# Optimization experiments

Hardware: AMD Instinct MI355X
Metric: run time of the kernel (lower is better)

The kernel has to match this reference:

```python
import jax, jax.numpy as jnp
import numpy as np

B, T, D, H = 2, 4096, 768, 12
HD = D // H  # head_dim = 64


def setup_inputs() -> dict:
    key = jax.random.key(0)
    ks = jax.random.split(key, 6)
    s = 0.02
    return {
        "x": jax.random.normal(ks[0], (B, T, D), dtype=jnp.float32),
        "Wq": jax.random.normal(ks[1], (D, D), dtype=jnp.float32) * s,
        "Wk": jax.random.normal(ks[2], (D, D), dtype=jnp.float32) * s,
        "Wv": jax.random.normal(ks[3], (D, D), dtype=jnp.float32) * s,
        "Wo": jax.random.normal(ks[4], (D, D), dtype=jnp.float32) * s,
        "bo": jnp.zeros((D,), dtype=jnp.float32),
    }


def reference(x, Wq, Wk, Wv, Wo, bo):
    b, t, d = x.shape
    # QKV projections (no bias), reshape to [B, H, T, HD]
    def heads(w):
        return (x @ w.T).reshape(b, t, H, HD).transpose(0, 2, 1, 3)
    q, k, v = heads(Wq), heads(Wk), heads(Wv)
    scores = jnp.einsum("bhqd,bhkd->bhqk", q, k)  # [B,H,T,T]
    causal = jnp.tril(jnp.ones((t, t), dtype=bool))
    scores = jnp.where(causal, scores, -jnp.inf)
    attn = jax.nn.softmax(scores / jnp.sqrt(jnp.float32(HD)), axis=-1)
    ctx = jnp.einsum("bhqk,bhkd->bhqd", attn, v)  # [B,H,T,HD]
    ctx = ctx.transpose(0, 2, 1, 3).reshape(b, t, d)
    return ctx @ Wo.T + bo
```

## Files before the change

kernel.cpp:

```cpp
#include <hip/hip_runtime.h>
#include <hip/hip_bf16.h>
#include <cstdint>
#include <cstddef>

#define B_  2
#define T_  4096
#define D_  768
#define H_  12
#define HD_ 64
#define M_  (B_*T_)

#define SCL 0.18033688f

typedef __bf16 bf16x8 __attribute__((ext_vector_type(8)));
typedef float  f32x4  __attribute__((ext_vector_type(4)));
using bf16 = __hip_bfloat16;

__device__ inline float fexp2(float x) {
  float r; asm("v_exp_f32 %0, %1" : "=v"(r) : "v"(x)); return r;
}
__device__ inline uint32_t fu(float x) { union { float f; uint32_t u; } c; c.f = x; return c.u; }
__device__ inline uint32_t pktr(float a, float b) {
  return __builtin_amdgcn_perm(fu(b), fu(a), 0x07060302);
}
#define GLD16(g, l) __builtin_amdgcn_global_load_lds( \
    (const __attribute__((address_space(1))) uint32_t*)(const void*)(g), \
    (__attribute__((address_space(3))) uint32_t*)(void*)(l), 16, 0, 0)

__global__ void cvt_all(const float* __restrict__ x,
                        const float* __restrict__ w0, const float* __restrict__ w1,
                        const float* __restrict__ w2, const float* __restrict__ w3,
                        bf16* __restrict__ xd,
                        bf16* __restrict__ d0, bf16* __restrict__ d1,
                        bf16* __restrict__ d2, bf16* __restrict__ d3) {
  int blk = blockIdx.x;
  const float* s; bf16* d; int i;
  if (blk < 6144) {
    s = x; d = xd; i = blk * 256 + threadIdx.x;
  } else {
    int q = blk - 6144, which = q / 576, rb = q % 576;
    switch (which) {
      case 0: s = w0; d = d0; break;
      case 1: s = w1; d = d1; break;
      case 2: s = w2; d = d2; break;
      default: s = w3; d = d3; break;
    }
    i = rb * 256 + threadIdx.x;
  }
  float4 v = ((const float4*)s)[i];
  union { bf16 o[4]; uint2 u; } pk;
  pk.o[0] = __float2bfloat16(v.x); pk.o[1] = __float2bfloat16(v.y);
  pk.o[2] = __float2bfloat16(v.z); pk.o[3] = __float2bfloat16(v.w);
  *(uint2*)(d + 4 * (size_t)i) = pk.u;
}

__global__ __launch_bounds__(256) void gemm_qkv(const bf16* __restrict__ x,
                                                const bf16* __restrict__ W0,
                                                const bf16* __restrict__ W1,
                                                const bf16* __restrict__ W2,
                                                bf16* __restrict__ O0,
                                                bf16* __restrict__ O1,
                                                bf16* __restrict__ O2t) {
  __shared__ bf16 As[2][4096];
  __shared__ bf16 Bs[2][4096];
  const int flat = blockIdx.x;
  const int by = flat / 18;
  const int rr = flat % 18;
  const int z  = rr / 6;
  const int bx = rr % 6;
  const bf16* Wz = (z == 0) ? W0 : ((z == 1) ? W1 : W2);
  const char* Ap; const char* Bp; int a0, b0;
  if (z == 2) { Ap = (const char*)x;  a0 = by * 128; Bp = (const char*)Wz; b0 = bx * 128; }
  else        { Ap = (const char*)Wz; a0 = bx * 128; Bp = (const char*)x;  b0 = by * 128; }
  const int t = threadIdx.x;
  const int w = t >> 6, lane = t & 63;
  const int wa = (w >> 1) * 64, wb = (w & 1) * 64;
  const int mi = lane & 15, qd = lane >> 4;

  int aoff[2], boff[2];
  #pragma unroll
  for (int i = 0; i < 2; ++i) {
    int L = i * 256 + t;
    int row = L >> 2, sl = L & 3, c = sl ^ (row & 3);
    aoff[i] = (a0 + row) * 1536 + c * 16;
    boff[i] = (b0 + row) * 1536 + c * 16;
  }
  const int fsw = (qd ^ (mi & 3)) * 8;

  f32x4 acc[4][4] = {};

  #pragma unroll
  for (int i = 0; i < 2; ++i) {
    GLD16(Ap + aoff[i], &As[0][i * 2048 + w * 512]);
    GLD16(Bp + boff[i], &Bs[0][i * 2048 + w * 512]);
  }

  for (int kk = 0; kk < 24; ++kk) {
    __syncthreads();
    const int par = kk & 1;
    if (kk + 1 < 24) {
      const int np = par ^ 1, kb = (kk + 1) * 64;
      #pragma unroll
      for (int i = 0; i < 2; ++i) {
        GLD16(Ap + aoff[i] + kb, &As[np][i * 2048 + w * 512]);
        GLD16(Bp + boff[i] + kb, &Bs[np][i * 2048 + w * 512]);
      }
    }
    bf16x8 af[4], bfr[4];
    #pragma unroll
    for (int at = 0; at < 4; ++at)
      af[at] = *(const bf16x8*)&As[par][(wa + at * 16 + mi) * 32 + fsw];
    #pragma unroll
    for (int bt = 0; bt < 4; ++bt)
      bfr[bt] = *(const bf16x8*)&Bs[par][(wb + bt * 16 + mi) * 32 + fsw];
    #pragma unroll
    for (int at = 0; at < 4; ++at)
      #pragma unroll
      for (int bt = 0; bt < 4; ++bt)
        acc[at][bt] = __builtin_amdgcn_mfma_f32_16x16x32_bf16(af[at], bfr[bt], acc[at][bt], 0, 0, 0);
  }

  if (z == 2) {
    #pragma unroll
    for (int at = 0; at < 4; ++at)
      #pragma unroll
      for (int bt = 0; bt < 4; ++bt) {
        int gr = a0 + wa + at * 16 + qd * 4;
        int gc = b0 + wb + bt * 16 + mi;
        union { bf16 o[4]; uint2 u; } pk;
        #pragma unroll
        for (int r = 0; r < 4; ++r) pk.o[r] = __float2bfloat16(acc[at][bt][r]);
        int bb = gr >> 12, tt = gr & 4095;
        *(uint2*)(O2t + (size_t)bb * 768 * 4096 + (size_t)gc * 4096 + tt) = pk.u;
      }
  } else {
    const float scl = (z == 1) ? SCL : 1.0f;
    bf16* Ob = (z == 0) ? O0 : O1;
    #pragma unroll
    for (int at = 0; at < 4; ++at)
      #pragma unroll
      for (int bt = 0; bt < 4; ++bt) {
        int f0  = a0 + wa + at * 16 + qd * 4;
        int tkn = b0 + wb + bt * 16 + mi;
        union { bf16 o[4]; uint2 u; } pk;
        #pragma unroll
        for (int r = 0; r < 4; ++r) pk.o[r] = __float2bfloat16(acc[at][bt][r] * scl);
        *(uint2*)(Ob + (size_t)tkn * 768 + f0) = pk.u;
      }
  }
}

__global__ __launch_bounds__(256) void gemm_out(const bf16* __restrict__ ctx,
                                                const bf16* __restrict__ Wo,
                                                float* __restrict__ Cf,
                                                const float* __restrict__ bias) {
  __shared__ bf16 As[2][4096];
  __shared__ bf16 Bs[2][4096];
  const int flat = blockIdx.x;
  const int by = flat / 6, bx = flat % 6;
  const char* Ap = (const char*)Wo;  const int a0 = bx * 128;
  const char* Bp = (const char*)ctx; const int b0 = by * 128;
  const int t = threadIdx.x;
  const int w = t >> 6, lane = t & 63;
  const int wa = (w >> 1) * 64, wb = (w & 1) * 64;
  const int mi = lane & 15, qd = lane >> 4;

  int aoff[2], boff[2];
  #pragma unroll
  for (int i = 0; i < 2; ++i) {
    int L = i * 256 + t;
    int row = L >> 2, sl = L & 3, c = sl ^ (row & 3);
    aoff[i] = (a0 + row) * 1536 + c * 16;
    boff[i] = (b0 + row) * 1536 + c * 16;
  }
  const int fsw = (qd ^ (mi & 3)) * 8;

  f32x4 acc[4][4] = {};

  #pragma unroll
  for (int i = 0; i < 2; ++i) {
    GLD16(Ap + aoff[i], &As[0][i * 2048 + w * 512]);
    GLD16(Bp + boff[i], &Bs[0][i * 2048 + w * 512]);
  }

  for (int kk = 0; kk < 24; ++kk) {
    __syncthreads();
    const int par = kk & 1;
    if (kk + 1 < 24) {
      const int np = par ^ 1, kb = (kk + 1) * 64;
      #pragma unroll
      for (int i = 0; i < 2; ++i) {
        GLD16(Ap + aoff[i] + kb, &As[np][i * 2048 + w * 512]);
        GLD16(Bp + boff[i] + kb, &Bs[np][i * 2048 + w * 512]);
      }
    }
    bf16x8 af[4], bfr[4];
    #pragma unroll
    for (int at = 0; at < 4; ++at)
      af[at] = *(const bf16x8*)&As[par][(wa + at * 16 + mi) * 32 + fsw];
    #pragma unroll
    for (int bt = 0; bt < 4; ++bt)
      bfr[bt] = *(const bf16x8*)&Bs[par][(wb + bt * 16 + mi) * 32 + fsw];
    #pragma unroll
    for (int at = 0; at < 4; ++at)
      #pragma unroll
      for (int bt = 0; bt < 4; ++bt)
        acc[at][bt] = __builtin_amdgcn_mfma_f32_16x16x32_bf16(af[at], bfr[bt], acc[at][bt], 0, 0, 0);
  }

  #pragma unroll
  for (int at = 0; at < 4; ++at)
    #pragma unroll
    for (int bt = 0; bt < 4; ++bt) {
      int f0  = a0 + wa + at * 16 + qd * 4;
      int tkn = b0 + wb + bt * 16 + mi;
      float4 bv = *(const float4*)&bias[f0];
      float4 o;
      o.x = acc[at][bt][0] + bv.x; o.y = acc[at][bt][1] + bv.y;
      o.z = acc[at][bt][2] + bv.z; o.w = acc[at][bt][3] + bv.w;
      *(float4*)&Cf[(size_t)tkn * 768 + f0] = o;
    }
}

__global__ __launch_bounds__(512, 4) void flash_attn(const bf16* __restrict__ Q,
                                                     const bf16* __restrict__ K,
                                                     const bf16* __restrict__ Vt,
                                                     bf16* __restrict__ ctx) {
  __shared__ bf16 Ks[2][4096];
  __shared__ bf16 Vs[2][4096];
  __shared__ bf16 Pt[8][16 * 72];
  const int t = threadIdx.x;
  const int w = t >> 6, lane = t & 63;
  const int mi = lane & 15, qd = lane >> 4;
  const int bh   = blockIdx.x % 24;
  const int qrev = blockIdx.x / 24;
  const int q0 = T_ - 128 - qrev * 128;
  const int b = bh / H_, h = bh % H_;
  const size_t bTD = (size_t)b * T_ * D_;
  const char* Kp = (const char*)(K  + bTD + (size_t)h * HD_);
  const char* Vp = (const char*)(Vt + (size_t)b * D_ * T_ + (size_t)h * HD_ * T_);
  const int qw = q0 + w * 16;

  const int rl = t >> 3, c = (t & 7) ^ (rl & 7);
  const int vkoff = rl * 1536 + c * 16;
  const int vvoff = rl * 8192 + c * 16;

  int fidx[4][2];
  #pragma unroll
  for (int jt = 0; jt < 4; ++jt)
    #pragma unroll
    for (int kt = 0; kt < 2; ++kt)
      fidx[jt][kt] = (jt * 16 + mi) * 64 + (((kt * 4 + qd) ^ (mi & 7)) * 8);

  bf16x8 qf[2];
  const bf16* Qp = Q + bTD + (size_t)h * HD_;
  #pragma unroll
  for (int kt = 0; kt < 2; ++kt)
    qf[kt] = *(const bf16x8*)(Qp + (size_t)(qw + mi) * D_ + kt * 32 + qd * 8);

  f32x4 oacc[4] = {};
  float lst = 0.f;
  const int ntiles = q0 / 64 + 2;

  GLD16(Kp + vkoff, &Ks[0][w * 512]);
  GLD16(Vp + vvoff, &Vs[0][w * 512]);

  for (int tt = 0; tt < ntiles; ++tt) {
    __syncthreads();
    const int par = tt & 1;
    if (tt + 1 < ntiles) {
      const size_t j1 = (size_t)(tt + 1) * 64;
      const int np = par ^ 1;
      GLD16(Kp + vkoff + j1 * 1536, &Ks[np][w * 512]);
      GLD16(Vp + vvoff + j1 * 2,    &Vs[np][w * 512]);
    }
    const int j0 = tt * 64;
    if (j0 > qw + 15) continue;

    f32x4 sacc[4] = {};
    #pragma unroll
    for (int jt = 0; jt < 4; ++jt)
      #pragma unroll
      for (int kt = 0; kt < 2; ++kt) {
        bf16x8 kf = *(const bf16x8*)&Ks[par][fidx[jt][kt]];
        sacc[jt] = __builtin_amdgcn_mfma_f32_16x16x32_bf16(kf, qf[kt], sacc[jt], 0, 0, 0);
      }

    if (j0 + 63 > qw) {
      const int qg = qw + mi;
      #pragma unroll
      for (int jt = 0; jt < 4; ++jt)
        #pragma unroll
        for (int r = 0; r < 4; ++r) {
          int jg = j0 + jt * 16 + qd * 4 + r;
          if (jg > qg) sacc[jt][r] = -1e30f;
        }
    }

    #pragma unroll
    for (int jt = 0; jt < 4; ++jt) {
      float p0 = fexp2(sacc[jt][0]);
      float p1 = fexp2(sacc[jt][1]);
      float p2 = fexp2(sacc[jt][2]);
      float p3 = fexp2(sacc[jt][3]);
      lst += (p0 + p1) + (p2 + p3);
      union { uint32_t u[2]; uint64_t d; } pw;
      pw.u[0] = pktr(p0, p1);
      pw.u[1] = pktr(p2, p3);
      *(uint64_t*)&Pt[w][mi * 72 + jt * 16 + qd * 4] = pw.d;
    }

    asm volatile("s_waitcnt lgkmcnt(0)" ::: "memory");

    #pragma unroll
    for (int ktp = 0; ktp < 2; ++ktp) {
      bf16x8 pfx = *(const bf16x8*)&Pt[w][mi * 72 + ktp * 32 + qd * 8];
      #pragma unroll
      for (int dt = 0; dt < 4; ++dt) {
        bf16x8 vf = *(const bf16x8*)&Vs[par][fidx[dt][ktp]];
        oacc[dt] = __builtin_amdgcn_mfma_f32_16x16x32_bf16(vf, pfx, oacc[dt], 0, 0, 0);
      }
    }
  }

  float l = lst;
  l += __shfl_xor(l, 16);
  l += __shfl_xor(l, 32);
  float inv = __builtin_amdgcn_rcpf(l);
  const int qg = qw + mi;
  bf16* cp = ctx + bTD + (size_t)qg * D_ + h * HD_ + qd * 4;
  #pragma unroll
  for (int dt = 0; dt < 4; ++dt) {
    union { bf16 o[4]; uint2 u; } pko;
    #pragma unroll
    for (int r = 0; r < 4; ++r) pko.o[r] = __float2bfloat16(oacc[dt][r] * inv);
    *(uint2*)(cp + dt * 16) = pko.u;
  }
}

extern "C" void kernel_launch(void* const* d_in, const int* in_sizes, int n_in,
                              void* d_out, int out_size, void* d_ws, size_t ws_size,
                              hipStream_t stream) {
  const float* x  = (const float*)d_in[0];
  const float* Wq = (const float*)d_in[1];
  const float* Wk = (const float*)d_in[2];
  const float* Wv = (const float*)d_in[3];
  const float* Wo = (const float*)d_in[4];
  const float* bo = (const float*)d_in[5];
  float* out = (float*)d_out;

  char* ws = (char*)d_ws;
  const size_t SZ  = (size_t)M_ * D_ * 2;
  const size_t WSZ = (size_t)D_ * D_ * 2;
  bf16* xb   = (bf16*)(ws);
  bf16* Qb   = (bf16*)(ws + 1 * SZ);
  bf16* Kb   = (bf16*)(ws + 2 * SZ);
  bf16* Vtg  = (bf16*)(ws + 3 * SZ);
  bf16* ctxb = (bf16*)(ws + 4 * SZ);
  bf16* Wqb  = (bf16*)(ws + 5 * SZ);
  bf16* Wkb  = (bf16*)(ws + 5 * SZ + 1 * WSZ);
  bf16* Wvb  = (bf16*)(ws + 5 * SZ + 2 * WSZ);
  bf16* Wob  = (bf16*)(ws + 5 * SZ + 3 * WSZ);

  cvt_all<<<6144 + 4 * 576, 256, 0, stream>>>(x, Wq, Wk, Wv, Wo, xb, Wqb, Wkb, Wvb, Wob);

  gemm_qkv<<<1152, 256, 0, stream>>>(xb, Wqb, Wkb, Wvb, Qb, Kb, Vtg);

  flash_attn<<<(T_ / 128) * B_ * H_, 512, 0, stream>>>(Qb, Kb, Vtg, ctxb);

  gemm_out<<<384, 256, 0, stream>>>(ctxb, Wob, out, bo);
}
```

Before: 245.7 us.

## Halve flash-attention block to 64 query rows with 4 waves and swizzled P buffer

Each flash-attention block now covers 64 query rows with 256 threads (4 waves) instead of 128 rows with 512 threads, which doubles the grid. Each thread issues two K/V tile loads, and the per-wave skip of fully masked tiles is removed, so every wave in a block now does the same work. The P staging buffer in shared memory uses an XOR-swizzled layout instead of a padded stride. This cuts causal-diagonal waste and evens out load across blocks, at the cost of fewer rows reusing each loaded K/V tile, which doubles K/V global traffic.

```diff
diff --git a/kernel.cpp b/kernel.cpp
--- a/kernel.cpp
+++ b/kernel.cpp
@@ -222,28 +222,33 @@
     }
 }
 
-__global__ __launch_bounds__(512, 4) void flash_attn(const bf16* __restrict__ Q,
+__global__ __launch_bounds__(256, 4) void flash_attn(const bf16* __restrict__ Q,
                                                      const bf16* __restrict__ K,
                                                      const bf16* __restrict__ Vt,
                                                      bf16* __restrict__ ctx) {
   __shared__ bf16 Ks[2][4096];
   __shared__ bf16 Vs[2][4096];
-  __shared__ bf16 Pt[8][16 * 72];
+  __shared__ bf16 Pt[4][1024];
   const int t = threadIdx.x;
   const int w = t >> 6, lane = t & 63;
   const int mi = lane & 15, qd = lane >> 4;
   const int bh   = blockIdx.x % 24;
   const int qrev = blockIdx.x / 24;
-  const int q0 = T_ - 128 - qrev * 128;
+  const int q0 = T_ - 64 - qrev * 64;
   const int b = bh / H_, h = bh % H_;
   const size_t bTD = (size_t)b * T_ * D_;
   const char* Kp = (const char*)(K  + bTD + (size_t)h * HD_);
   const char* Vp = (const char*)(Vt + (size_t)b * D_ * T_ + (size_t)h * HD_ * T_);
   const int qw = q0 + w * 16;
 
-  const int rl = t >> 3, c = (t & 7) ^ (rl & 7);
-  const int vkoff = rl * 1536 + c * 16;
-  const int vvoff = rl * 8192 + c * 16;
+  int vkoff[2], vvoff[2];
+  #pragma unroll
+  for (int i = 0; i < 2; ++i) {
+    int L = i * 256 + t;
+    int rl = L >> 3, c = (L & 7) ^ (rl & 7);
+    vkoff[i] = rl * 1536 + c * 16;
+    vvoff[i] = rl * 8192 + c * 16;
+  }
 
   int fidx[4][2];
   #pragma unroll
@@ -252,6 +257,14 @@
     for (int kt = 0; kt < 2; ++kt)
       fidx[jt][kt] = (jt * 16 + mi) * 64 + (((kt * 4 + qd) ^ (mi & 7)) * 8);
 
+  int pwoff[4], proff[2];
+  #pragma unroll
+  for (int jt = 0; jt < 4; ++jt)
+    pwoff[jt] = mi * 64 + ((2 * jt + (qd >> 1)) ^ (mi & 7)) * 8 + (qd & 1) * 4;
+  #pragma unroll
+  for (int kt = 0; kt < 2; ++kt)
+    proff[kt] = mi * 64 + ((4 * kt + qd) ^ (mi & 7)) * 8;
+
   bf16x8 qf[2];
   const bf16* Qp = Q + bTD + (size_t)h * HD_;
   #pragma unroll
@@ -260,10 +273,13 @@
 
   f32x4 oacc[4] = {};
   float lst = 0.f;
-  const int ntiles = q0 / 64 + 2;
-
-  GLD16(Kp + vkoff, &Ks[0][w * 512]);
-  GLD16(Vp + vvoff, &Vs[0][w * 512]);
+  const int ntiles = q0 / 64 + 1;
+
+  #pragma unroll
+  for (int i = 0; i < 2; ++i) {
+    GLD16(Kp + vkoff[i], &Ks[0][i * 2048 + w * 512]);
+    GLD16(Vp + vvoff[i], &Vs[0][i * 2048 + w * 512]);
+  }
 
   for (int tt = 0; tt < ntiles; ++tt) {
     __syncthreads();
@@ -271,11 +287,13 @@
     if (tt + 1 < ntiles) {
       const size_t j1 = (size_t)(tt + 1) * 64;
       const int np = par ^ 1;
-      GLD16(Kp + vkoff + j1 * 1536, &Ks[np][w * 512]);
-      GLD16(Vp + vvoff + j1 * 2,    &Vs[np][w * 512]);
+      #pragma unroll
+      for (int i = 0; i < 2; ++i) {
+        GLD16(Kp + vkoff[i] + j1 * 1536, &Ks[np][i * 2048 + w * 512]);
+        GLD16(Vp + vvoff[i] + j1 * 2,    &Vs[np][i * 2048 + w * 512]);
+      }
     }
     const int j0 = tt * 64;
-    if (j0 > qw + 15) continue;
 
     f32x4 sacc[4] = {};
     #pragma unroll
@@ -307,14 +325,14 @@
       union { uint32_t u[2]; uint64_t d; } pw;
       pw.u[0] = pktr(p0, p1);
       pw.u[1] = pktr(p2, p3);
-      *(uint64_t*)&Pt[w][mi * 72 + jt * 16 + qd * 4] = pw.d;
+      *(uint64_t*)&Pt[w][pwoff[jt]] = pw.d;
     }
 
     asm volatile("s_waitcnt lgkmcnt(0)" ::: "memory");
 
     #pragma unroll
     for (int ktp = 0; ktp < 2; ++ktp) {
-      bf16x8 pfx = *(const bf16x8*)&Pt[w][mi * 72 + ktp * 32 + qd * 8];
+      bf16x8 pfx = *(const bf16x8*)&Pt[w][proff[ktp]];
       #pragma unroll
       for (int dt = 0; dt < 4; ++dt) {
         bf16x8 vf = *(const bf16x8*)&Vs[par][fidx[dt][ktp]];
@@ -366,7 +384,7 @@
 
   gemm_qkv<<<1152, 256, 0, stream>>>(xb, Wqb, Wkb, Wvb, Qb, Kb, Vtg);
 
-  flash_attn<<<(T_ / 128) * B_ * H_, 512, 0, stream>>>(Qb, Kb, Vtg, ctxb);
+  flash_attn<<<(T_ / 64) * B_ * H_, 256, 0, stream>>>(Qb, Kb, Vtg, ctxb);
 
   gemm_out<<<384, 256, 0, stream>>>(ctxb, Wob, out, bo);
 }
```

Measured after the change: 244.0 us. No clear change (-0.7%).
